# Kernel optimization log

Hardware: AMD Instinct MI355X
Metric: run time of the kernel (lower is better)

## Reference

```python
import jax, jax.numpy as jnp
import numpy as np

NUM_HEADS = 12
HEAD_DIM = 64


def setup_inputs() -> dict:
    key = jax.random.key(0)
    ks = jax.random.split(key, 8)
    B, S, D, M = 8, 1024, 768, 8
    scale = 0.02
    return {
        "hidden_states": jax.random.normal(ks[0], (B, S, D), jnp.float32),
        "memory": jax.random.normal(ks[1], (1, M, D), jnp.float32) * scale,
        "Wq": jax.random.normal(ks[2], (D, D), jnp.float32) * scale,
        "bq": jnp.zeros((D,), jnp.float32),
        "Wk": jax.random.normal(ks[3], (D, D), jnp.float32) * scale,
        "bk": jnp.zeros((D,), jnp.float32),
        "Wv": jax.random.normal(ks[4], (D, D), jnp.float32) * scale,
        "bv": jnp.zeros((D,), jnp.float32),
    }


def _split_heads(x):
    # (B, S, D) -> (B, H, S, Dh)
    B, S, _ = x.shape
    return x.reshape(B, S, NUM_HEADS, HEAD_DIM).transpose(0, 2, 1, 3)


def reference(hidden_states, memory, Wq, bq, Wk, bk, Wv, bv):
    B, S, D = hidden_states.shape
    # prepend? no: memory tokens are concatenated AFTER hidden_states on token dim
    mem = jnp.broadcast_to(memory, (B,) + memory.shape[1:])
    with_memory = jnp.concatenate([hidden_states, mem], axis=1)  # (B, S+M, D)

    # torch nn.Linear: x @ W.T + b
    q = _split_heads(hidden_states @ Wq.T + bq)   # (B, H, S,   Dh)
    k = _split_heads(with_memory @ Wk.T + bk)     # (B, H, S+M, Dh)
    v = _split_heads(with_memory @ Wv.T + bv)     # (B, H, S+M, Dh)

    scaling = 1.0 / np.sqrt(HEAD_DIM).astype(np.float32)
    scores = jnp.einsum("bhqd,bhkd->bhqk", q, k) * scaling
    probs = jax.nn.softmax(scores, axis=-1)  # dropout is identity in eval
    ctx = jnp.einsum("bhqk,bhkd->bhqd", probs, v)  # (B, H, S, Dh)
    ctx = ctx.transpose(0, 2, 1, 3).reshape(B, S, D)
    return ctx
```

## Files before the change

### kernel.cpp

```cpp
#include <hip/hip_runtime.h>

typedef unsigned short ushort_t;
typedef __attribute__((ext_vector_type(8))) short bf16x8;
typedef __attribute__((ext_vector_type(4))) short s16x4;
typedef __attribute__((ext_vector_type(4))) float f32x4;

#define BATCH 8
#define SEQ   1024
#define MEMT  8
#define LREAL 1032
#define LPAD  1152
#define DMODEL 768
#define NH    12
#define DH    64

__device__ __forceinline__ ushort_t f2b(float x) {
  union { float f; unsigned u; } c; c.f = x;
  unsigned u = c.u;
  unsigned r = (u + 0x7fffu + ((u >> 16) & 1u)) >> 16;
  return (ushort_t)r;
}

#if defined(__has_builtin)
#if __has_builtin(__builtin_amdgcn_global_load_lds)
#define HAVE_GLL 1
#endif
#if __has_builtin(__builtin_amdgcn_exp2f)
#define EXP2F(x) __builtin_amdgcn_exp2f(x)
#endif
#endif
#ifndef EXP2F
#define EXP2F(x) __expf((x) * 0.6931471805599453f)
#endif

#define CEXP 0.18033688011112042f

__device__ __forceinline__ void stage16(const ushort_t* g, ushort_t* lds_wave_base) {
#ifdef HAVE_GLL
  __builtin_amdgcn_global_load_lds(
      (const __attribute__((address_space(1))) unsigned int*)g,
      (__attribute__((address_space(3))) unsigned int*)lds_wave_base,
      16, 0, 0);
#else
  int lane = threadIdx.x & 63;
  *(bf16x8*)(lds_wave_base + lane * 8) = *(const bf16x8*)g;
#endif
}

__global__ __launch_bounds__(256) void build_xm(const float* __restrict__ hidden,
                                                const float* __restrict__ memv,
                                                ushort_t* __restrict__ Xm) {
  size_t idx = ((size_t)blockIdx.x * 256 + threadIdx.x) * 4;
  const size_t perB = (size_t)LPAD * DMODEL;
  int b = (int)(idx / perB);
  size_t rem = idx - (size_t)b * perB;
  int row = (int)(rem / DMODEL);
  int col = (int)(rem - (size_t)row * DMODEL);
  f32x4 v;
  if (row < SEQ) {
    v = *(const f32x4*)(hidden + ((size_t)b * SEQ + row) * DMODEL + col);
  } else if (row < LREAL) {
    v = *(const f32x4*)(memv + (size_t)(row - SEQ) * DMODEL + col);
  } else {
    v = (f32x4){0.f, 0.f, 0.f, 0.f};
  }
  s16x4 p;
  p[0] = (short)f2b(v[0]); p[1] = (short)f2b(v[1]);
  p[2] = (short)f2b(v[2]); p[3] = (short)f2b(v[3]);
  *(s16x4*)(Xm + idx) = p;
}

__global__ __launch_bounds__(256) void cast3(const float* __restrict__ Wq,
                                             const float* __restrict__ Wk,
                                             const float* __restrict__ Wv,
                                             ushort_t* __restrict__ dq,
                                             ushort_t* __restrict__ dk,
                                             ushort_t* __restrict__ dv) {
  int i = blockIdx.x * 256 + threadIdx.x;
  const float* src = blockIdx.y == 0 ? Wq : (blockIdx.y == 1 ? Wk : Wv);
  ushort_t* dst = blockIdx.y == 0 ? dq : (blockIdx.y == 1 ? dk : dv);
  f32x4 v = *(const f32x4*)(src + (size_t)i * 4);
  s16x4 p;
  p[0] = (short)f2b(v[0]); p[1] = (short)f2b(v[1]);
  p[2] = (short)f2b(v[2]); p[3] = (short)f2b(v[3]);
  *(s16x4*)(dst + (size_t)i * 4) = p;
}

__global__ __launch_bounds__(256) void gemm_fused(
    const ushort_t* __restrict__ Xm,
    const ushort_t* __restrict__ Wqb, const ushort_t* __restrict__ Wkb,
    const ushort_t* __restrict__ Wvb,
    const float* __restrict__ bq, const float* __restrict__ bk,
    const float* __restrict__ bv,
    ushort_t* __restrict__ Qb, ushort_t* __restrict__ Kb,
    ushort_t* __restrict__ Vtb) {
  __shared__ __align__(16) ushort_t As[128 * 32];
  __shared__ __align__(16) ushort_t Bs[128 * 32];
  const int tid = threadIdx.x;
  const int wave = tid >> 6, lane = tid & 63;
  const int quad = lane >> 4, l15 = lane & 15;
  const int wm = wave >> 1, wn = wave & 1;
  const int x = blockIdx.x, y = blockIdx.y, b = blockIdx.z;
  const ushort_t* Xb = Xm + (size_t)b * LPAD * DMODEL;

  const ushort_t *A, *W;
  const float* bias;
  int task, rowTile;
  const int colTile = x * 128;
  if (y < 6) {
    task = 2; A = Wvb; W = Xb; bias = bv; rowTile = y * 128;
  } else if (y < 14) {
    if (x >= 6) return;
    task = 0; A = Xb; W = Wqb; bias = bq; rowTile = (y - 6) * 128;
  } else {
    if (x >= 6) return;
    task = 1; A = Xb; W = Wkb; bias = bk; rowTile = (y - 14) * 128;
  }

  f32x4 acc[4][4] = {};

  for (int k0 = 0; k0 < DMODEL; k0 += 32) {
#pragma unroll
    for (int is = 0; is < 2; ++is) {
      int cw = is * 256 + wave * 64;
      int c = cw + lane;
      int r = c >> 2, cc = (c & 3) << 3;
      stage16(A + (size_t)(rowTile + r) * DMODEL + k0 + cc, As + cw * 8);
      stage16(W + (size_t)(colTile + r) * DMODEL + k0 + cc, Bs + cw * 8);
    }
    __syncthreads();
    bf16x8 af[4], bfr[4];
#pragma unroll
    for (int mt = 0; mt < 4; ++mt)
      af[mt] = *(const bf16x8*)&As[(wm * 64 + mt * 16 + l15) * 32 + quad * 8];
#pragma unroll
    for (int nt = 0; nt < 4; ++nt)
      bfr[nt] = *(const bf16x8*)&Bs[(wn * 64 + nt * 16 + l15) * 32 + quad * 8];
#pragma unroll
    for (int mt = 0; mt < 4; ++mt)
#pragma unroll
      for (int nt = 0; nt < 4; ++nt)
        acc[mt][nt] = __builtin_amdgcn_mfma_f32_16x16x32_bf16(af[mt], bfr[nt], acc[mt][nt], 0, 0, 0);
    __syncthreads();
  }

  if (task == 2) {
#pragma unroll
    for (int mt = 0; mt < 4; ++mt) {
      int row0 = rowTile + wm * 64 + mt * 16 + quad * 4;
      float bvr[4];
#pragma unroll
      for (int r = 0; r < 4; ++r) bvr[r] = bias[row0 + r];
#pragma unroll
      for (int nt = 0; nt < 4; ++nt) {
        int col = colTile + wn * 64 + nt * 16 + l15;
#pragma unroll
        for (int r = 0; r < 4; ++r) {
          int row = row0 + r;
          Vtb[(((size_t)b * NH + (row >> 6)) * DH + (row & 63)) * LPAD + col] =
              f2b(acc[mt][nt][r] + bvr[r]);
        }
      }
    }
  } else {
    ushort_t* out = task == 0 ? Qb : Kb;
    const int Rows = task == 0 ? SEQ : LPAD;
#pragma unroll
    for (int mt = 0; mt < 4; ++mt)
#pragma unroll
      for (int nt = 0; nt < 4; ++nt) {
        int row0 = rowTile + wm * 64 + mt * 16 + quad * 4;
        int col = colTile + wn * 64 + nt * 16 + l15;
        int h = col >> 6, d = col & 63;
        float bsv = bias[col];
#pragma unroll
        for (int r = 0; r < 4; ++r)
          out[(((size_t)b * NH + h) * Rows + (row0 + r)) * DH + d] = f2b(acc[mt][nt][r] + bsv);
      }
  }
}

__global__ __launch_bounds__(256, 3) void attn(const ushort_t* __restrict__ Q,
                                               const ushort_t* __restrict__ K,
                                               const ushort_t* __restrict__ Vt,
                                               float* __restrict__ Out) {
  __shared__ __align__(16) ushort_t Ks[4096];
  __shared__ __align__(16) ushort_t Vs[4096];
  __shared__ __align__(16) ushort_t Ps[4 * 2304];

  const int tid = threadIdx.x, wave = tid >> 6, lane = tid & 63;
  const int quad = lane >> 4, l15 = lane & 15;
  const int qt = blockIdx.x, h = blockIdx.y, b = blockIdx.z;

  const ushort_t* Qp = Q + (((size_t)b * NH + h) * SEQ + qt * 128) * DH;
  const ushort_t* Kp = K + ((size_t)b * NH + h) * LPAD * DH;
  const ushort_t* Vp = Vt + ((size_t)b * NH + h) * DH * LPAD;
  ushort_t* Pw = Ps + wave * 2304;

  bf16x8 qf[2][2];
#pragma unroll
  for (int mt = 0; mt < 2; ++mt)
#pragma unroll
    for (int kk = 0; kk < 2; ++kk)
      qf[mt][kk] = *(const bf16x8*)&Qp[(wave * 32 + mt * 16 + l15) * DH + kk * 32 + quad * 8];

  f32x4 ob[2][4] = {};
  float lrow[2][4] = {};

  const int srow = tid >> 2;
  const int soff = (tid & 3) << 3;

  for (int kt = 0; kt < 17; ++kt) {
    const int key0 = kt * 64;
#pragma unroll
    for (int p = 0; p < 2; ++p) {
      stage16(Kp + (size_t)(key0 + srow) * DH + p * 32 + soff,
              Ks + p * 2048 + wave * 512);
      stage16(Vp + (size_t)srow * LPAD + key0 + p * 32 + soff,
              Vs + p * 2048 + wave * 512);
    }
    __syncthreads();

    f32x4 sc[2][4] = {};
#pragma unroll
    for (int kk = 0; kk < 2; ++kk)
#pragma unroll
      for (int nt = 0; nt < 4; ++nt) {
        bf16x8 kf = *(const bf16x8*)&Ks[kk * 2048 + (nt * 16 + l15) * 32 + quad * 8];
#pragma unroll
        for (int mt = 0; mt < 2; ++mt)
          sc[mt][nt] = __builtin_amdgcn_mfma_f32_16x16x32_bf16(qf[mt][kk], kf, sc[mt][nt], 0, 0, 0);
      }

    const bool lastTile = (kt == 16);
    const bool colValid = (l15 < 8);
#pragma unroll
    for (int mt = 0; mt < 2; ++mt)
#pragma unroll
      for (int nt = 0; nt < 4; ++nt) {
#pragma unroll
        for (int r = 0; r < 4; ++r) {
          float pv = EXP2F(sc[mt][nt][r] * CEXP);
          if (lastTile && !(nt == 0 && colValid)) pv = 0.f;
          union { float f; unsigned u; } cu; cu.f = pv;
          unsigned t = cu.u + 0x7fffu + ((cu.u >> 16) & 1u);
          unsigned hi = t & 0xffff0000u;
          union { unsigned u; float f; } cb; cb.u = hi;
          lrow[mt][r] += cb.f;
          Pw[(mt * 16 + quad * 4 + r) * 72 + nt * 16 + l15] = (ushort_t)(t >> 16);
        }
      }

#pragma unroll
    for (int kk = 0; kk < 2; ++kk) {
      bf16x8 pf[2];
#pragma unroll
      for (int mt = 0; mt < 2; ++mt)
        pf[mt] = *(const bf16x8*)&Pw[(mt * 16 + l15) * 72 + kk * 32 + quad * 8];
#pragma unroll
      for (int dt = 0; dt < 4; ++dt) {
        bf16x8 vf = *(const bf16x8*)&Vs[kk * 2048 + (dt * 16 + l15) * 32 + quad * 8];
#pragma unroll
        for (int mt = 0; mt < 2; ++mt)
          ob[mt][dt] = __builtin_amdgcn_mfma_f32_16x16x32_bf16(pf[mt], vf, ob[mt][dt], 0, 0, 0);
      }
    }
    __syncthreads();
  }

#pragma unroll
  for (int mt = 0; mt < 2; ++mt)
#pragma unroll
    for (int r = 0; r < 4; ++r) {
      float s = lrow[mt][r];
      s += __shfl_xor(s, 1, 16);
      s += __shfl_xor(s, 2, 16);
      s += __shfl_xor(s, 4, 16);
      s += __shfl_xor(s, 8, 16);
      lrow[mt][r] = 1.0f / s;
    }

#pragma unroll
  for (int mt = 0; mt < 2; ++mt) {
    int row0 = qt * 128 + wave * 32 + mt * 16 + quad * 4;
#pragma unroll
    for (int dt = 0; dt < 4; ++dt) {
      int col = h * DH + dt * 16 + l15;
#pragma unroll
      for (int r = 0; r < 4; ++r)
        Out[((size_t)b * SEQ + row0 + r) * DMODEL + col] = ob[mt][dt][r] * lrow[mt][r];
    }
  }
}

extern "C" void kernel_launch(void* const* d_in, const int* in_sizes, int n_in,
                              void* d_out, int out_size, void* d_ws, size_t ws_size,
                              hipStream_t stream) {
  const float* hidden = (const float*)d_in[0];
  const float* memv   = (const float*)d_in[1];
  const float* Wq = (const float*)d_in[2];
  const float* bq = (const float*)d_in[3];
  const float* Wk = (const float*)d_in[4];
  const float* bk = (const float*)d_in[5];
  const float* Wv = (const float*)d_in[6];
  const float* bv = (const float*)d_in[7];
  float* out = (float*)d_out;

  char* ws = (char*)d_ws;
  size_t off = 0;
  ushort_t* Xm  = (ushort_t*)(ws + off); off += (size_t)BATCH * LPAD * DMODEL * 2;
  ushort_t* Wqb = (ushort_t*)(ws + off); off += (size_t)DMODEL * DMODEL * 2;
  ushort_t* Wkb = (ushort_t*)(ws + off); off += (size_t)DMODEL * DMODEL * 2;
  ushort_t* Wvb = (ushort_t*)(ws + off); off += (size_t)DMODEL * DMODEL * 2;
  ushort_t* Qb  = (ushort_t*)(ws + off); off += (size_t)BATCH * NH * SEQ * DH * 2;
  ushort_t* Kb  = (ushort_t*)(ws + off); off += (size_t)BATCH * NH * LPAD * DH * 2;
  ushort_t* Vtb = (ushort_t*)(ws + off);

  build_xm<<<dim3(BATCH * LPAD * DMODEL / 4 / 256), 256, 0, stream>>>(hidden, memv, Xm);
  cast3<<<dim3(DMODEL * DMODEL / 4 / 256, 3), 256, 0, stream>>>(Wq, Wk, Wv, Wqb, Wkb, Wvb);
  gemm_fused<<<dim3(9, 23, 8), 256, 0, stream>>>(Xm, Wqb, Wkb, Wvb, bq, bk, bv, Qb, Kb, Vtb);
  attn<<<dim3(SEQ / 128, NH, BATCH), 256, 0, stream>>>(Qb, Kb, Vtb, out);
}
```

Baseline: 198.7 us.

## Merge prep kernels, remap GEMM grid, fold softmax scale, widen attention key tiles

Combines the activation and weight bf16 cast kernels into one launch. Flattens the projection GEMM grid so no blocks exit early, with a block order that spreads work across chiplets, and doubles the K-step per barrier. Folds the softmax exp2 scale into Q at projection time. In attention it processes 128 keys per barrier, computes row sums with an MFMA against a ones vector instead of per-element adds plus shuffles, and truncates P to bf16 instead of rounding it. These changes aim to cut launch overhead, barrier count and VALU work, at the cost of extra LDS per block and slightly different rounding.

```diff
diff --git a/kernel.cpp b/kernel.cpp
--- a/kernel.cpp
+++ b/kernel.cpp
@@ -14,6 +14,8 @@
 #define NH    12
 #define DH    64
 
+#define CEXP 0.18033688011112042f
+
 __device__ __forceinline__ ushort_t f2b(float x) {
   union { float f; unsigned u; } c; c.f = x;
   unsigned u = c.u;
@@ -32,8 +34,6 @@
 #ifndef EXP2F
 #define EXP2F(x) __expf((x) * 0.6931471805599453f)
 #endif
-
-#define CEXP 0.18033688011112042f
 
 __device__ __forceinline__ void stage16(const ushort_t* g, ushort_t* lds_wave_base) {
 #ifdef HAVE_GLL
@@ -47,43 +47,47 @@
 #endif
 }
 
-__global__ __launch_bounds__(256) void build_xm(const float* __restrict__ hidden,
-                                                const float* __restrict__ memv,
-                                                ushort_t* __restrict__ Xm) {
-  size_t idx = ((size_t)blockIdx.x * 256 + threadIdx.x) * 4;
-  const size_t perB = (size_t)LPAD * DMODEL;
-  int b = (int)(idx / perB);
-  size_t rem = idx - (size_t)b * perB;
-  int row = (int)(rem / DMODEL);
-  int col = (int)(rem - (size_t)row * DMODEL);
-  f32x4 v;
-  if (row < SEQ) {
-    v = *(const f32x4*)(hidden + ((size_t)b * SEQ + row) * DMODEL + col);
-  } else if (row < LREAL) {
-    v = *(const f32x4*)(memv + (size_t)(row - SEQ) * DMODEL + col);
+__global__ __launch_bounds__(256) void prep(const float* __restrict__ hidden,
+                                            const float* __restrict__ memv,
+                                            const float* __restrict__ Wq,
+                                            const float* __restrict__ Wk,
+                                            const float* __restrict__ Wv,
+                                            ushort_t* __restrict__ Xm,
+                                            ushort_t* __restrict__ Wqb,
+                                            ushort_t* __restrict__ Wkb,
+                                            ushort_t* __restrict__ Wvb) {
+  int bx = blockIdx.x;
+  if (bx < 6912) {
+    size_t idx = ((size_t)bx * 256 + threadIdx.x) * 4;
+    const size_t perB = (size_t)LPAD * DMODEL;
+    int b = (int)(idx / perB);
+    size_t rem = idx - (size_t)b * perB;
+    int row = (int)(rem / DMODEL);
+    int col = (int)(rem - (size_t)row * DMODEL);
+    f32x4 v;
+    if (row < SEQ) {
+      v = *(const f32x4*)(hidden + ((size_t)b * SEQ + row) * DMODEL + col);
+    } else if (row < LREAL) {
+      v = *(const f32x4*)(memv + (size_t)(row - SEQ) * DMODEL + col);
+    } else {
+      v = (f32x4){0.f, 0.f, 0.f, 0.f};
+    }
+    s16x4 p;
+    p[0] = (short)f2b(v[0]); p[1] = (short)f2b(v[1]);
+    p[2] = (short)f2b(v[2]); p[3] = (short)f2b(v[3]);
+    *(s16x4*)(Xm + idx) = p;
   } else {
-    v = (f32x4){0.f, 0.f, 0.f, 0.f};
-  }
-  s16x4 p;
-  p[0] = (short)f2b(v[0]); p[1] = (short)f2b(v[1]);
-  p[2] = (short)f2b(v[2]); p[3] = (short)f2b(v[3]);
-  *(s16x4*)(Xm + idx) = p;
-}
-
-__global__ __launch_bounds__(256) void cast3(const float* __restrict__ Wq,
-                                             const float* __restrict__ Wk,
-                                             const float* __restrict__ Wv,
-                                             ushort_t* __restrict__ dq,
-                                             ushort_t* __restrict__ dk,
-                                             ushort_t* __restrict__ dv) {
-  int i = blockIdx.x * 256 + threadIdx.x;
-  const float* src = blockIdx.y == 0 ? Wq : (blockIdx.y == 1 ? Wk : Wv);
-  ushort_t* dst = blockIdx.y == 0 ? dq : (blockIdx.y == 1 ? dk : dv);
-  f32x4 v = *(const f32x4*)(src + (size_t)i * 4);
-  s16x4 p;
-  p[0] = (short)f2b(v[0]); p[1] = (short)f2b(v[1]);
-  p[2] = (short)f2b(v[2]); p[3] = (short)f2b(v[3]);
-  *(s16x4*)(dst + (size_t)i * 4) = p;
+    int t = bx - 6912;
+    int m = t / 576;
+    int i = (t - m * 576) * 256 + threadIdx.x;
+    const float* src = m == 0 ? Wq : (m == 1 ? Wk : Wv);
+    ushort_t* dst = m == 0 ? Wqb : (m == 1 ? Wkb : Wvb);
+    f32x4 v = *(const f32x4*)(src + (size_t)i * 4);
+    s16x4 p;
+    p[0] = (short)f2b(v[0]); p[1] = (short)f2b(v[1]);
+    p[2] = (short)f2b(v[2]); p[3] = (short)f2b(v[3]);
+    *(s16x4*)(dst + (size_t)i * 4) = p;
+  }
 }
 
 __global__ __launch_bounds__(256) void gemm_fused(
@@ -94,53 +98,70 @@
     const float* __restrict__ bv,
     ushort_t* __restrict__ Qb, ushort_t* __restrict__ Kb,
     ushort_t* __restrict__ Vtb) {
-  __shared__ __align__(16) ushort_t As[128 * 32];
-  __shared__ __align__(16) ushort_t Bs[128 * 32];
+  __shared__ __align__(16) ushort_t As[2 * 4096];
+  __shared__ __align__(16) ushort_t Bs[2 * 4096];
   const int tid = threadIdx.x;
   const int wave = tid >> 6, lane = tid & 63;
   const int quad = lane >> 4, l15 = lane & 15;
   const int wm = wave >> 1, wn = wave & 1;
-  const int x = blockIdx.x, y = blockIdx.y, b = blockIdx.z;
+
+  int bx = blockIdx.x;
+  int task, xt, yt, b;
+  if (bx < 432) {
+    int slot = bx & 7, rest = bx >> 3;
+    int y = rest % 6, vhi = rest / 6;
+    int v = slot + 8 * vhi;
+    task = 2; xt = v % 9; b = v / 9; yt = y;
+  } else if (bx < 816) {
+    int t = bx - 432;
+    int slot = t & 7, rest = t >> 3;
+    int x = rest % 6, qhi = rest / 6;
+    int q = slot + 8 * qhi;
+    task = 0; xt = x; yt = q & 7; b = q >> 3;
+  } else {
+    int t = bx - 816;
+    int slot = t & 7, rest = t >> 3;
+    int x = rest % 6, khi = rest / 6;
+    int k = slot + 8 * khi;
+    task = 1; xt = x; yt = k % 9; b = k / 9;
+  }
+  const int rowTile = yt * 128, colTile = xt * 128;
   const ushort_t* Xb = Xm + (size_t)b * LPAD * DMODEL;
-
-  const ushort_t *A, *W;
-  const float* bias;
-  int task, rowTile;
-  const int colTile = x * 128;
-  if (y < 6) {
-    task = 2; A = Wvb; W = Xb; bias = bv; rowTile = y * 128;
-  } else if (y < 14) {
-    if (x >= 6) return;
-    task = 0; A = Xb; W = Wqb; bias = bq; rowTile = (y - 6) * 128;
-  } else {
-    if (x >= 6) return;
-    task = 1; A = Xb; W = Wkb; bias = bk; rowTile = (y - 14) * 128;
-  }
+  const ushort_t* A = task == 2 ? Wvb : Xb;
+  const ushort_t* W = task == 2 ? Xb : (task == 0 ? Wqb : Wkb);
+  const float* bias = task == 2 ? bv : (task == 0 ? bq : bk);
+
+  const int srow = tid >> 2;
+  const int scol = (tid & 3) << 3;
 
   f32x4 acc[4][4] = {};
 
-  for (int k0 = 0; k0 < DMODEL; k0 += 32) {
-#pragma unroll
-    for (int is = 0; is < 2; ++is) {
-      int cw = is * 256 + wave * 64;
-      int c = cw + lane;
-      int r = c >> 2, cc = (c & 3) << 3;
-      stage16(A + (size_t)(rowTile + r) * DMODEL + k0 + cc, As + cw * 8);
-      stage16(W + (size_t)(colTile + r) * DMODEL + k0 + cc, Bs + cw * 8);
-    }
+  for (int k0 = 0; k0 < DMODEL; k0 += 64) {
+#pragma unroll
+    for (int kk = 0; kk < 2; ++kk)
+#pragma unroll
+      for (int is = 0; is < 2; ++is) {
+        int r = is * 64 + srow;
+        int lb = kk * 4096 + is * 2048 + wave * 512;
+        stage16(A + (size_t)(rowTile + r) * DMODEL + k0 + kk * 32 + scol, As + lb);
+        stage16(W + (size_t)(colTile + r) * DMODEL + k0 + kk * 32 + scol, Bs + lb);
+      }
     __syncthreads();
-    bf16x8 af[4], bfr[4];
-#pragma unroll
-    for (int mt = 0; mt < 4; ++mt)
-      af[mt] = *(const bf16x8*)&As[(wm * 64 + mt * 16 + l15) * 32 + quad * 8];
-#pragma unroll
-    for (int nt = 0; nt < 4; ++nt)
-      bfr[nt] = *(const bf16x8*)&Bs[(wn * 64 + nt * 16 + l15) * 32 + quad * 8];
-#pragma unroll
-    for (int mt = 0; mt < 4; ++mt)
+#pragma unroll
+    for (int kk = 0; kk < 2; ++kk) {
+      bf16x8 af[4], bfr[4];
+#pragma unroll
+      for (int mt = 0; mt < 4; ++mt)
+        af[mt] = *(const bf16x8*)&As[kk * 4096 + (wm * 64 + mt * 16 + l15) * 32 + quad * 8];
 #pragma unroll
       for (int nt = 0; nt < 4; ++nt)
-        acc[mt][nt] = __builtin_amdgcn_mfma_f32_16x16x32_bf16(af[mt], bfr[nt], acc[mt][nt], 0, 0, 0);
+        bfr[nt] = *(const bf16x8*)&Bs[kk * 4096 + (wn * 64 + nt * 16 + l15) * 32 + quad * 8];
+#pragma unroll
+      for (int mt = 0; mt < 4; ++mt)
+#pragma unroll
+        for (int nt = 0; nt < 4; ++nt)
+          acc[mt][nt] = __builtin_amdgcn_mfma_f32_16x16x32_bf16(af[mt], bfr[nt], acc[mt][nt], 0, 0, 0);
+    }
     __syncthreads();
   }
 
@@ -165,6 +186,7 @@
   } else {
     ushort_t* out = task == 0 ? Qb : Kb;
     const int Rows = task == 0 ? SEQ : LPAD;
+    const float scale = task == 0 ? CEXP : 1.0f;
 #pragma unroll
     for (int mt = 0; mt < 4; ++mt)
 #pragma unroll
@@ -175,7 +197,8 @@
         float bsv = bias[col];
 #pragma unroll
         for (int r = 0; r < 4; ++r)
-          out[(((size_t)b * NH + h) * Rows + (row0 + r)) * DH + d] = f2b(acc[mt][nt][r] + bsv);
+          out[(((size_t)b * NH + h) * Rows + (row0 + r)) * DH + d] =
+              f2b((acc[mt][nt][r] + bsv) * scale);
       }
   }
 }
@@ -184,13 +207,14 @@
                                                const ushort_t* __restrict__ K,
                                                const ushort_t* __restrict__ Vt,
                                                float* __restrict__ Out) {
-  __shared__ __align__(16) ushort_t Ks[4096];
-  __shared__ __align__(16) ushort_t Vs[4096];
+  __shared__ __align__(16) ushort_t Ks[2 * 4096];
+  __shared__ __align__(16) ushort_t Vs[4 * 2048];
   __shared__ __align__(16) ushort_t Ps[4 * 2304];
 
   const int tid = threadIdx.x, wave = tid >> 6, lane = tid & 63;
   const int quad = lane >> 4, l15 = lane & 15;
-  const int qt = blockIdx.x, h = blockIdx.y, b = blockIdx.z;
+  const int bh = blockIdx.x, qt = blockIdx.y;
+  const int h = bh % NH, b = bh / NH;
 
   const ushort_t* Qp = Q + (((size_t)b * NH + h) * SEQ + qt * 128) * DH;
   const ushort_t* Kp = K + ((size_t)b * NH + h) * LPAD * DH;
@@ -204,91 +228,106 @@
     for (int kk = 0; kk < 2; ++kk)
       qf[mt][kk] = *(const bf16x8*)&Qp[(wave * 32 + mt * 16 + l15) * DH + kk * 32 + quad * 8];
 
+  bf16x8 ones8;
+#pragma unroll
+  for (int j = 0; j < 8; ++j) ones8[j] = (short)0x3f80;
+
   f32x4 ob[2][4] = {};
-  float lrow[2][4] = {};
+  f32x4 obl[2] = {};
 
   const int srow = tid >> 2;
-  const int soff = (tid & 3) << 3;
-
-  for (int kt = 0; kt < 17; ++kt) {
-    const int key0 = kt * 64;
-#pragma unroll
-    for (int p = 0; p < 2; ++p) {
-      stage16(Kp + (size_t)(key0 + srow) * DH + p * 32 + soff,
-              Ks + p * 2048 + wave * 512);
-      stage16(Vp + (size_t)srow * LPAD + key0 + p * 32 + soff,
-              Vs + p * 2048 + wave * 512);
-    }
+  const int scol = (tid & 3) << 3;
+
+  for (int kt = 0; kt < 9; ++kt) {
+    const int key0 = kt * 128;
+#pragma unroll
+    for (int kk = 0; kk < 2; ++kk)
+#pragma unroll
+      for (int is = 0; is < 2; ++is) {
+        int krow = is * 64 + srow;
+        stage16(Kp + (size_t)(key0 + krow) * DH + kk * 32 + scol,
+                Ks + kk * 4096 + is * 2048 + wave * 512);
+      }
+#pragma unroll
+    for (int kc = 0; kc < 4; ++kc)
+      stage16(Vp + (size_t)srow * LPAD + key0 + kc * 32 + scol,
+              Vs + kc * 2048 + wave * 512);
     __syncthreads();
 
-    f32x4 sc[2][4] = {};
-#pragma unroll
-    for (int kk = 0; kk < 2; ++kk)
-#pragma unroll
-      for (int nt = 0; nt < 4; ++nt) {
-        bf16x8 kf = *(const bf16x8*)&Ks[kk * 2048 + (nt * 16 + l15) * 32 + quad * 8];
+#pragma unroll
+    for (int half = 0; half < 2; ++half) {
+      f32x4 sc[2][4] = {};
+#pragma unroll
+      for (int kk = 0; kk < 2; ++kk)
+#pragma unroll
+        for (int nt = 0; nt < 4; ++nt) {
+          bf16x8 kf = *(const bf16x8*)&Ks[kk * 4096 + (half * 64 + nt * 16 + l15) * 32 + quad * 8];
+#pragma unroll
+          for (int mt = 0; mt < 2; ++mt)
+            sc[mt][nt] = __builtin_amdgcn_mfma_f32_16x16x32_bf16(qf[mt][kk], kf, sc[mt][nt], 0, 0, 0);
+        }
+
+      if (kt < 8) {
 #pragma unroll
         for (int mt = 0; mt < 2; ++mt)
-          sc[mt][nt] = __builtin_amdgcn_mfma_f32_16x16x32_bf16(qf[mt][kk], kf, sc[mt][nt], 0, 0, 0);
-      }
-
-    const bool lastTile = (kt == 16);
-    const bool colValid = (l15 < 8);
-#pragma unroll
-    for (int mt = 0; mt < 2; ++mt)
-#pragma unroll
-      for (int nt = 0; nt < 4; ++nt) {
-#pragma unroll
-        for (int r = 0; r < 4; ++r) {
-          float pv = EXP2F(sc[mt][nt][r] * CEXP);
-          if (lastTile && !(nt == 0 && colValid)) pv = 0.f;
-          union { float f; unsigned u; } cu; cu.f = pv;
-          unsigned t = cu.u + 0x7fffu + ((cu.u >> 16) & 1u);
-          unsigned hi = t & 0xffff0000u;
-          union { unsigned u; float f; } cb; cb.u = hi;
-          lrow[mt][r] += cb.f;
-          Pw[(mt * 16 + quad * 4 + r) * 72 + nt * 16 + l15] = (ushort_t)(t >> 16);
+#pragma unroll
+          for (int nt = 0; nt < 4; ++nt)
+#pragma unroll
+            for (int r = 0; r < 4; ++r) {
+              union { float f; unsigned u; } cu;
+              cu.f = EXP2F(sc[mt][nt][r]);
+              Pw[(mt * 16 + quad * 4 + r) * 72 + nt * 16 + l15] = (ushort_t)(cu.u >> 16);
+            }
+      } else {
+#pragma unroll
+        for (int mt = 0; mt < 2; ++mt)
+#pragma unroll
+          for (int nt = 0; nt < 4; ++nt) {
+            int key = key0 + half * 64 + nt * 16 + l15;
+            bool valid = key < LREAL;
+#pragma unroll
+            for (int r = 0; r < 4; ++r) {
+              union { float f; unsigned u; } cu;
+              cu.f = valid ? EXP2F(sc[mt][nt][r]) : 0.f;
+              Pw[(mt * 16 + quad * 4 + r) * 72 + nt * 16 + l15] = (ushort_t)(cu.u >> 16);
+            }
+          }
+      }
+
+#pragma unroll
+      for (int kc2 = 0; kc2 < 2; ++kc2) {
+        int kcg = half * 2 + kc2;
+        bf16x8 pf[2];
+#pragma unroll
+        for (int mt = 0; mt < 2; ++mt)
+          pf[mt] = *(const bf16x8*)&Pw[(mt * 16 + l15) * 72 + kc2 * 32 + quad * 8];
+#pragma unroll
+        for (int dt = 0; dt < 4; ++dt) {
+          bf16x8 vf = *(const bf16x8*)&Vs[kcg * 2048 + (dt * 16 + l15) * 32 + quad * 8];
+#pragma unroll
+          for (int mt = 0; mt < 2; ++mt)
+            ob[mt][dt] = __builtin_amdgcn_mfma_f32_16x16x32_bf16(pf[mt], vf, ob[mt][dt], 0, 0, 0);
         }
-      }
-
-#pragma unroll
-    for (int kk = 0; kk < 2; ++kk) {
-      bf16x8 pf[2];
-#pragma unroll
-      for (int mt = 0; mt < 2; ++mt)
-        pf[mt] = *(const bf16x8*)&Pw[(mt * 16 + l15) * 72 + kk * 32 + quad * 8];
-#pragma unroll
-      for (int dt = 0; dt < 4; ++dt) {
-        bf16x8 vf = *(const bf16x8*)&Vs[kk * 2048 + (dt * 16 + l15) * 32 + quad * 8];
 #pragma unroll
         for (int mt = 0; mt < 2; ++mt)
-          ob[mt][dt] = __builtin_amdgcn_mfma_f32_16x16x32_bf16(pf[mt], vf, ob[mt][dt], 0, 0, 0);
+          obl[mt] = __builtin_amdgcn_mfma_f32_16x16x32_bf16(pf[mt], ones8, obl[mt], 0, 0, 0);
       }
     }
     __syncthreads();
   }
-
-#pragma unroll
-  for (int mt = 0; mt < 2; ++mt)
-#pragma unroll
-    for (int r = 0; r < 4; ++r) {
-      float s = lrow[mt][r];
-      s += __shfl_xor(s, 1, 16);
-      s += __shfl_xor(s, 2, 16);
-      s += __shfl_xor(s, 4, 16);
-      s += __shfl_xor(s, 8, 16);
-      lrow[mt][r] = 1.0f / s;
-    }
 
 #pragma unroll
   for (int mt = 0; mt < 2; ++mt) {
     int row0 = qt * 128 + wave * 32 + mt * 16 + quad * 4;
+    f32x4 linv;
+#pragma unroll
+    for (int r = 0; r < 4; ++r) linv[r] = 1.0f / obl[mt][r];
 #pragma unroll
     for (int dt = 0; dt < 4; ++dt) {
       int col = h * DH + dt * 16 + l15;
 #pragma unroll
       for (int r = 0; r < 4; ++r)
-        Out[((size_t)b * SEQ + row0 + r) * DMODEL + col] = ob[mt][dt][r] * lrow[mt][r];
+        Out[((size_t)b * SEQ + row0 + r) * DMODEL + col] = ob[mt][dt][r] * linv[r];
     }
   }
 }
@@ -316,8 +355,7 @@
   ushort_t* Kb  = (ushort_t*)(ws + off); off += (size_t)BATCH * NH * LPAD * DH * 2;
   ushort_t* Vtb = (ushort_t*)(ws + off);
 
-  build_xm<<<dim3(BATCH * LPAD * DMODEL / 4 / 256), 256, 0, stream>>>(hidden, memv, Xm);
-  cast3<<<dim3(DMODEL * DMODEL / 4 / 256, 3), 256, 0, stream>>>(Wq, Wk, Wv, Wqb, Wkb, Wvb);
-  gemm_fused<<<dim3(9, 23, 8), 256, 0, stream>>>(Xm, Wqb, Wkb, Wvb, bq, bk, bv, Qb, Kb, Vtb);
-  attn<<<dim3(SEQ / 128, NH, BATCH), 256, 0, stream>>>(Qb, Kb, Vtb, out);
-}
+  prep<<<dim3(8640), 256, 0, stream>>>(hidden, memv, Wq, Wk, Wv, Xm, Wqb, Wkb, Wvb);
+  gemm_fused<<<dim3(1248), 256, 0, stream>>>(Xm, Wqb, Wkb, Wvb, bq, bk, bv, Qb, Kb, Vtb);
+  attn<<<dim3(96, 8), 256, 0, stream>>>(Qb, Kb, Vtb, out);
+}
```

New measurement: 186.1 us. 6.3% less time.
